# Performance work log

Measured on AMD Instinct MI355X. Metric: run time of the kernel, lower is better.

## Reference

```python
import jax, jax.numpy as jnp
import numpy as np

# Dims: B=4, C_in=256, H=W=64 -> L=4096, token_dim D=256, state_dim N=512, K=4
B_, C_IN, H_, W_ = 4, 256, 64, 64
D, N, K = 256, 512, 4


def setup_inputs() -> dict:
    key = jax.random.key(0)
    ks = jax.random.split(key, 16)
    g = lambda k, shape, sc=0.02: (jax.random.normal(k, shape, jnp.float32) * sc)
    return {
        'feat_map': jax.random.normal(ks[0], (B_, C_IN, H_, W_), jnp.float32),
        'hf_map':   jax.random.normal(ks[1], (B_, C_IN, H_, W_), jnp.float32),
        # 1x1 conv proj_f / proj_hf: weight (out=D, in=C_IN), bias (D,)
        'Wf':  g(ks[2], (D, C_IN)), 'bf':  jnp.zeros((D,), jnp.float32),
        'Whf': g(ks[3], (D, C_IN)), 'bhf': jnp.zeros((D,), jnp.float32),
        # alpha_head: Linear(D, D//2) -> GELU -> Linear(D//2, K)
        'Wa1': g(ks[4], (D // 2, D)), 'ba1': jnp.zeros((D // 2,), jnp.float32),
        'Wa2': g(ks[5], (K, D // 2)), 'ba2': jnp.zeros((K,), jnp.float32),
        # SelectiveSSM base tuples: diagonal decay logits A (K,N), input maps B (K,N,D), output maps C (K,D,N)
        'A_base': g(ks[6], (K, N), 1.0),
        'B_base': g(ks[7], (K, N, D), 0.02),
        'C_base': g(ks[8], (K, D, N), 0.02),
        # out_proj 1x1 conv: (C_IN, D)
        'Wout': g(ks[9], (C_IN, D)), 'bout': jnp.zeros((C_IN,), jnp.float32),
    }


def _stage(feat_map, hf_map, Wf, bf, Whf, bhf, Wa1, ba1, Wa2, ba2,
           A_base, B_base, C_base, Wout, bout):
    B, C, H, W = feat_map.shape
    L = H * W
    # 1x1 conv token projections -> (B, L, D)
    t_f = jnp.einsum('bchw,dc->bdhw', feat_map, Wf) + bf[None, :, None, None]
    t_hf = jnp.einsum('bchw,dc->bdhw', hf_map, Whf) + bhf[None, :, None, None]
    x = t_f.reshape(B, -1, L).transpose(0, 2, 1)        # (B, L, D)
    t_hf_seq = t_hf.reshape(B, -1, L).transpose(0, 2, 1)  # (B, L, D)
    # gating MLP -> per-token mixture weights over K base SSMs
    hmid = jax.nn.gelu(t_hf_seq @ Wa1.T + ba1, approximate=False)
    alpha = jax.nn.softmax(hmid @ Wa2.T + ba2, axis=-1)  # (B, L, K)
    # selective SSM: per-token mixed diagonal decay and input drive
    a = jax.nn.sigmoid(jnp.einsum('blk,kn->bln', alpha, A_base))   # (B, L, N)
    u = jnp.einsum('bld,blk,knd->bln', x, alpha, B_base)           # (B, L, N)

    def step(h, au):
        a_t, u_t = au                   # each (B, N)
        h = a_t * h + u_t
        return h, h

    h0 = jnp.zeros((B, a.shape[-1]), x.dtype)
    _, hs = jax.lax.scan(step, h0, (a.transpose(1, 0, 2), u.transpose(1, 0, 2)))
    h_seq = hs.transpose(1, 0, 2)                                   # (B, L, N)
    # mixed readout
    y = jnp.einsum('blk,bln,kdn->bld', alpha, h_seq, C_base)        # (B, L, D)
    y_map = y.transpose(0, 2, 1).reshape(B, -1, H, W)
    out = jnp.einsum('bdhw,cd->bchw', y_map, Wout) + bout[None, :, None, None]
    return out


def reference(feat_map, hf_map, Wf, bf, Whf, bhf, Wa1, ba1, Wa2, ba2,
              A_base, B_base, C_base, Wout, bout):
    return _stage(feat_map, hf_map, Wf, bf, Whf, bhf, Wa1, ba1, Wa2, ba2,
                  A_base, B_base, C_base, Wout, bout)
```

## Files before the change

kernel.cpp:

```cpp
#include <hip/hip_runtime.h>
#include <hip/hip_bf16.h>
#include <math.h>

#define B_  4
#define CIN 256
#define L_  4096
#define D_  256
#define N_  512
#define K_  4
#define DH  128
#define BL  (B_ * L_)

#define NCHUNK 128
#define CLEN   (L_ / NCHUNK)

typedef __attribute__((ext_vector_type(8))) short bfrag;
typedef __attribute__((ext_vector_type(4))) float f4;

__device__ __forceinline__ float bf2f(unsigned short u) {
  return __uint_as_float(((unsigned int)u) << 16);
}
__device__ __forceinline__ unsigned short f2bf(float f) {
  unsigned int u = __float_as_uint(f);
  return (unsigned short)((u + 0x7FFFu + ((u >> 16) & 1u)) >> 16);
}

__global__ void k_prep(const float* __restrict__ Wf, const float* __restrict__ Whf,
                       const float* __restrict__ Wa1, const float* __restrict__ Wout,
                       const float* __restrict__ Bb, const float* __restrict__ Cb,
                       const float* __restrict__ bfv, const float* __restrict__ bhfv,
                       unsigned short* __restrict__ Wfb ,
                       unsigned short* __restrict__ Wa1b,
                       unsigned short* __restrict__ Woutb,
                       unsigned short* __restrict__ Bb16,
                       unsigned short* __restrict__ Cb16,
                       float* __restrict__ biascat) {
  int i = blockIdx.x * 256 + threadIdx.x;
  if (i < 65536) { Wfb[i] = f2bf(Wf[i]); return; } i -= 65536;
  if (i < 65536) { Wfb[65536 + i] = f2bf(Whf[i]); return; } i -= 65536;
  if (i < 32768) { Wa1b[i] = f2bf(Wa1[i]); return; } i -= 32768;
  if (i < 65536) { Woutb[i] = f2bf(Wout[i]); return; } i -= 65536;
  if (i < 524288) {
    int d = i & 255, n = (i >> 8) & 511, k = i >> 17;
    Bb16[(((size_t)n << 2) | k) << 8 | d] = f2bf(Bb[i]);
    return;
  } i -= 524288;
  if (i < 524288) {
    int nn = i & 511, d = (i >> 9) & 255, k = i >> 17;
    Cb16[(((size_t)d << 2) | k) << 9 | nn] = f2bf(Cb[i]);
    return;
  } i -= 524288;
  if (i < 256) { biascat[i] = bfv[i]; return; } i -= 256;
  if (i < 256) { biascat[256 + i] = bhfv[i]; }
}

__global__ void k_transpose2(const float* __restrict__ feat, const float* __restrict__ hf,
                             unsigned short* __restrict__ featT ) {
  __shared__ float tile[32][33];
  const int z = blockIdx.z;
  const int b = z & 3, which = z >> 2;
  const float* in = which ? hf : feat;
  unsigned short* outT = featT + (size_t)which * BL * CIN;
  const int l0 = blockIdx.x * 32, c0 = blockIdx.y * 32;
  const int tx = threadIdx.x, ty = threadIdx.y;
  const float* p = in + ((size_t)b * CIN + c0 + ty) * L_ + l0 + tx;
#pragma unroll
  for (int i = 0; i < 32; i += 8) tile[ty + i][tx] = p[(size_t)i * L_];
  __syncthreads();
  unsigned short* q = outT + ((size_t)b * L_ + l0 + ty) * CIN + c0 + tx;
#pragma unroll
  for (int i = 0; i < 32; i += 8) q[(size_t)i * CIN] = f2bf(tile[tx][ty + i]);
}


__global__ void k_scanA(const unsigned short* __restrict__ u, const float* __restrict__ alpha,
                        const float* __restrict__ Abase,
                        float* __restrict__ P, float* __restrict__ Hend) {
  const int n = threadIdx.x;
  const int bc = blockIdx.x;
  const int b = bc >> 7, c = bc & 127;
  const float A0 = Abase[n], A1 = Abase[N_ + n], A2 = Abase[2 * N_ + n], A3 = Abase[3 * N_ + n];
  const size_t tok0 = (size_t)b * L_ + (size_t)c * CLEN;
  float p = 1.f, h = 0.f;
  for (int l = 0; l < CLEN; ++l) {
    const size_t t = tok0 + l;
    float4 al = *(const float4*)(alpha + t * 4);
    float s = al.x * A0 + al.y * A1 + al.z * A2 + al.w * A3;
    float av = 1.f / (1.f + expf(-s));
    float uv = bf2f(u[t * N_ + n]);
    h = av * h + uv;
    p *= av;
  }
  P[(size_t)bc * N_ + n] = p;
  Hend[(size_t)bc * N_ + n] = h;
}

__global__ void k_scanB(const float* __restrict__ P, const float* __restrict__ Hend,
                        float* __restrict__ Hstart) {
  const int n = threadIdx.x;
  const int b = blockIdx.x;
  float h = 0.f;
  for (int c = 0; c < NCHUNK; ++c) {
    size_t idx = ((size_t)b * NCHUNK + c) * N_ + n;
    Hstart[idx] = h;
    h = P[idx] * h + Hend[idx];
  }
}

__global__ void k_scanC(const unsigned short* __restrict__ u, const float* __restrict__ alpha,
                        const float* __restrict__ Abase, const float* __restrict__ Hstart,
                        unsigned short* __restrict__ hbf) {
  const int n = threadIdx.x;
  const int bc = blockIdx.x;
  const int b = bc >> 7, c = bc & 127;
  const float A0 = Abase[n], A1 = Abase[N_ + n], A2 = Abase[2 * N_ + n], A3 = Abase[3 * N_ + n];
  const size_t tok0 = (size_t)b * L_ + (size_t)c * CLEN;
  float h = Hstart[(size_t)bc * N_ + n];
  for (int l = 0; l < CLEN; ++l) {
    const size_t t = tok0 + l;
    float4 al = *(const float4*)(alpha + t * 4);
    float s = al.x * A0 + al.y * A1 + al.z * A2 + al.w * A3;
    float av = 1.f / (1.f + expf(-s));
    float uv = bf2f(u[t * N_ + n]);
    h = av * h + uv;
    hbf[t * N_ + n] = f2bf(h);
  }
}

#define BM 128
#define BN 128
#define BK 32

#define GLL(src, dst)                                                                      \
  __builtin_amdgcn_global_load_lds((const __attribute__((address_space(1))) void*)(src),   \
                                   (__attribute__((address_space(3))) void*)(dst), 16, 0, 0)

#define BM2 128
#define BN2 256

template <int BIAS, int EPI>
__global__ __launch_bounds__(512, 2) void gemm_bt2(
    const unsigned short* __restrict__ A, long sA,
    const unsigned short* __restrict__ Bm, long sB,
    const float* __restrict__ bias, long bS,
    const float* __restrict__ alphaP,
    void* __restrict__ Cv, long sC,
    int M, int N, int Kd, int lda, int ldb) {
  const int zb = blockIdx.z;
  A += (size_t)zb * sA;
  Bm += (size_t)zb * sB;
  if (BIAS) bias += (size_t)zb * bS;
  const int m0 = blockIdx.x * BM2;
  const int n0 = blockIdx.y * BN2;
  __shared__ __attribute__((aligned(16))) unsigned short As[2 * BM2 * BK];
  __shared__ __attribute__((aligned(16))) unsigned short Bs[2 * BN2 * BK];
  const int t = threadIdx.x;
  const int lane = t & 63;
  const int w = t >> 6;
  const int wm = (w >> 2) * 64;
  const int wn = (w & 3) * 64;

  f4 acc[4][4];
#pragma unroll
  for (int i = 0; i < 4; ++i)
#pragma unroll
    for (int j = 0; j < 4; ++j) acc[i][j] = (f4){0.f, 0.f, 0.f, 0.f};

  const int rS = t >> 2;
  const int cS = (((t & 3) ^ ((t >> 3) & 3))) * 8;
  const unsigned short* gA = A + (size_t)(m0 + rS) * lda + cS;
  const unsigned short* gB = Bm + (size_t)(n0 + rS) * ldb + cS;
  const long rowStepB = (long)128 * ldb;
  const int r16 = lane & 15;
  const int sx = (r16 >> 1) & 3;
  const int kg = (((lane >> 4) ^ sx)) * 8;

#define STAGE2(slot, kt)                                                \
  do {                                                                  \
    const unsigned short* sA_ = gA + (size_t)(kt) * BK;                 \
    const unsigned short* sB_ = gB + (size_t)(kt) * BK;                 \
    unsigned short* dA_ = As + (slot) * (BM2 * BK) + t * 8;             \
    unsigned short* dB_ = Bs + (slot) * (BN2 * BK) + t * 8;             \
    GLL(sA_, dA_);                                                      \
    GLL(sB_, dB_);                                                      \
    GLL(sB_ + rowStepB, dB_ + BM2 * BK);                                \
  } while (0)

  const int nIter = Kd / BK;
  STAGE2(0, 0);
  int cur = 0;
  for (int kt = 0; kt < nIter; ++kt) {
    asm volatile("s_waitcnt vmcnt(0)" ::: "memory");
    __builtin_amdgcn_s_barrier();
    asm volatile("" ::: "memory");
    if (kt + 1 < nIter) STAGE2(cur ^ 1, kt + 1);
    const unsigned short* Ab = As + cur * (BM2 * BK);
    const unsigned short* Bb2 = Bs + cur * (BN2 * BK);
    bfrag af[4], bfr[4];
#pragma unroll
    for (int i = 0; i < 4; ++i) {
      af[i]  = *(const bfrag*)(Ab + (wm + i * 16 + r16) * BK + kg);
      bfr[i] = *(const bfrag*)(Bb2 + (wn + i * 16 + r16) * BK + kg);
    }
    __builtin_amdgcn_s_setprio(1);
#pragma unroll
    for (int i = 0; i < 4; ++i)
#pragma unroll
      for (int j = 0; j < 4; ++j)
        acc[i][j] = __builtin_amdgcn_mfma_f32_16x16x32_bf16(af[i], bfr[j], acc[i][j], 0, 0, 0);
    __builtin_amdgcn_s_setprio(0);
    asm volatile("" ::: "memory");
    cur ^= 1;
  }
#undef STAGE2

  const int rowBase = m0 + wm + ((lane >> 4) << 2);
  const int colBase = n0 + wn + (lane & 15);

  if (EPI >= 2) {
    const int kq = lane & 3;
    const int NO = N >> 2;
    float av[4][4];
#pragma unroll
    for (int i = 0; i < 4; ++i)
#pragma unroll
      for (int r = 0; r < 4; ++r)
        av[i][r] = alphaP[(size_t)(rowBase + i * 16 + r) * 4 + kq];
    float* Cf = (float*)Cv + (size_t)zb * sC;
    unsigned short* Cb = (unsigned short*)Cv + (size_t)zb * sC;
#pragma unroll
    for (int i = 0; i < 4; ++i)
#pragma unroll
      for (int j = 0; j < 4; ++j) {
        const int col = colBase + j * 16;
#pragma unroll
        for (int r = 0; r < 4; ++r) {
          float p = av[i][r] * acc[i][j][r];
          p += __shfl_xor(p, 1);
          p += __shfl_xor(p, 2);
          if (kq == 0) {
            const int row = rowBase + i * 16 + r;
            if (EPI == 2) Cf[(size_t)row * NO + (col >> 2)] = p;
            else          Cb[(size_t)row * NO + (col >> 2)] = f2bf(p);
          }
        }
      }
    return;
  }

  float* Cf = (float*)Cv + (size_t)zb * sC;
  unsigned short* Cb = (unsigned short*)Cv + (size_t)zb * sC;
#pragma unroll
  for (int i = 0; i < 4; ++i) {
#pragma unroll
    for (int j = 0; j < 4; ++j) {
      const int col = colBase + j * 16;
#pragma unroll
      for (int r = 0; r < 4; ++r) {
        const int row = rowBase + i * 16 + r;
        float v = acc[i][j][r];
        if (BIAS == 1) v += bias[col];
        if (BIAS == 2) v += bias[row];
        if (EPI == 1) Cb[(size_t)row * N + col] = f2bf(v);
        else          Cf[(size_t)row * N + col] = v;
      }
    }
  }
}

template <int BIAS, int EPI >
__global__ __launch_bounds__(512, 2) void gemm_w8(
    const unsigned short* __restrict__ A, long sA,
    const unsigned short* __restrict__ Bm, long sB,
    const float* __restrict__ bias, long bS,
    void* __restrict__ Cv, long sC,
    int M, int N, int Kd, int lda, int ldb) {
  const int zb = blockIdx.z;
  A += (size_t)zb * sA;
  Bm += (size_t)zb * sB;
  if (BIAS) bias += (size_t)zb * bS;
  const int m0 = blockIdx.x * BM;
  const int n0 = blockIdx.y * BN;
  __shared__ __attribute__((aligned(16))) unsigned short As[3 * BM * BK];
  __shared__ __attribute__((aligned(16))) unsigned short Bs[3 * BN * BK];
  const int t = threadIdx.x;
  const int lane = t & 63;
  const int w = t >> 6;
  const int wm = (w >> 2) * 64;
  const int wn = (w & 3) * 32;

  f4 acc[4][2];
#pragma unroll
  for (int i = 0; i < 4; ++i)
#pragma unroll
    for (int j = 0; j < 2; ++j) acc[i][j] = (f4){0.f, 0.f, 0.f, 0.f};

  const int rS = t >> 2;
  const int cS = (((t & 3) ^ ((t >> 3) & 3))) * 8;
  const unsigned short* gA = A + (size_t)(m0 + rS) * lda + cS;
  const unsigned short* gB = Bm + (size_t)(n0 + rS) * ldb + cS;
  const int r16 = lane & 15;
  const int sx = (r16 >> 1) & 3;
  const int kg = (((lane >> 4) ^ sx)) * 8;

#define STAGEW(slot, kt)                                                \
  do {                                                                  \
    GLL(gA + (size_t)(kt) * BK, As + (slot) * (BM * BK) + t * 8);       \
    GLL(gB + (size_t)(kt) * BK, Bs + (slot) * (BN * BK) + t * 8);       \
  } while (0)

  const int nIter = Kd / BK;
  STAGEW(0, 0);
  STAGEW(1, 1);
  int slot = 0;
  for (int kt = 0; kt < nIter; ++kt) {
    if (kt + 1 < nIter) asm volatile("s_waitcnt vmcnt(2)" ::: "memory");
    else                asm volatile("s_waitcnt vmcnt(0)" ::: "memory");
    __builtin_amdgcn_s_barrier();
    asm volatile("" ::: "memory");
    if (kt + 2 < nIter) {
      int s2 = slot + 2; if (s2 >= 3) s2 -= 3;
      STAGEW(s2, kt + 2);
    }
    const unsigned short* Ab = As + slot * (BM * BK);
    const unsigned short* Bb2 = Bs + slot * (BN * BK);
    bfrag af[4], bfr[2];
#pragma unroll
    for (int i = 0; i < 4; ++i)
      af[i]  = *(const bfrag*)(Ab + (wm + i * 16 + r16) * BK + kg);
#pragma unroll
    for (int j = 0; j < 2; ++j)
      bfr[j] = *(const bfrag*)(Bb2 + (wn + j * 16 + r16) * BK + kg);
    __builtin_amdgcn_s_setprio(1);
#pragma unroll
    for (int i = 0; i < 4; ++i)
#pragma unroll
      for (int j = 0; j < 2; ++j)
        acc[i][j] = __builtin_amdgcn_mfma_f32_16x16x32_bf16(af[i], bfr[j], acc[i][j], 0, 0, 0);
    __builtin_amdgcn_s_setprio(0);
    asm volatile("" ::: "memory");
    slot = (slot == 2) ? 0 : slot + 1;
  }
#undef STAGEW

  const int rowBase = m0 + wm + ((lane >> 4) << 2);
  const int colBase = n0 + wn + (lane & 15);
  float* Cf = (float*)Cv + (size_t)zb * sC;
  unsigned short* Cb = (unsigned short*)Cv + (size_t)zb * sC;
#pragma unroll
  for (int i = 0; i < 4; ++i) {
#pragma unroll
    for (int j = 0; j < 2; ++j) {
      const int col = colBase + j * 16;
#pragma unroll
      for (int r = 0; r < 4; ++r) {
        const int row = rowBase + i * 16 + r;
        float v = acc[i][j][r];
        if (BIAS == 1) v += bias[col];
        if (BIAS == 2) v += bias[row];
        if (EPI == 1) Cb[(size_t)row * N + col] = f2bf(v);
        else          Cf[(size_t)row * N + col] = v;
      }
    }
  }
}

__global__ __launch_bounds__(512, 2) void gemm_alpha(
    const unsigned short* __restrict__ A,
    const unsigned short* __restrict__ Bm,
    const float* __restrict__ ba1, const float* __restrict__ Wa2,
    const float* __restrict__ ba2, float* __restrict__ alphaOut) {
  __shared__ __attribute__((aligned(16))) unsigned short smem[6 * BM * BK + 1344];
  unsigned short* As = smem;
  unsigned short* Bs = smem + 3 * BM * BK;
  unsigned short* tile = smem;
  float* w2s = (float*)(smem + 6 * BM * BK);
  float* b1s = w2s + 512;
  float* b2s = b1s + 128;
  const int t = threadIdx.x;
  const int lane = t & 63;
  const int w = t >> 6;
  const int wm = (w >> 2) * 64;
  const int wn = (w & 3) * 32;
  const int m0 = blockIdx.x * BM;

  f4 acc[4][2];
#pragma unroll
  for (int i = 0; i < 4; ++i)
#pragma unroll
    for (int j = 0; j < 2; ++j) acc[i][j] = (f4){0.f, 0.f, 0.f, 0.f};

  const int rS = t >> 2;
  const int cS = (((t & 3) ^ ((t >> 3) & 3))) * 8;
  const unsigned short* gA = A + (size_t)(m0 + rS) * D_ + cS;
  const unsigned short* gB = Bm + (size_t)rS * D_ + cS;
  const int r16 = lane & 15;
  const int sx = (r16 >> 1) & 3;
  const int kg = (((lane >> 4) ^ sx)) * 8;

#define STAGEA(slot, kt)                                                \
  do {                                                                  \
    GLL(gA + (size_t)(kt) * BK, As + (slot) * (BM * BK) + t * 8);       \
    GLL(gB + (size_t)(kt) * BK, Bs + (slot) * (BM * BK) + t * 8);       \
  } while (0)

  const int nIter = D_ / BK;
  STAGEA(0, 0);
  STAGEA(1, 1);
  int slot = 0;
  for (int kt = 0; kt < nIter; ++kt) {
    if (kt + 1 < nIter) asm volatile("s_waitcnt vmcnt(2)" ::: "memory");
    else                asm volatile("s_waitcnt vmcnt(0)" ::: "memory");
    __builtin_amdgcn_s_barrier();
    asm volatile("" ::: "memory");
    if (kt + 2 < nIter) {
      int s2 = slot + 2; if (s2 >= 3) s2 -= 3;
      STAGEA(s2, kt + 2);
    }
    const unsigned short* Ab = As + slot * (BM * BK);
    const unsigned short* Bb2 = Bs + slot * (BM * BK);
    bfrag af[4], bfr[2];
#pragma unroll
    for (int i = 0; i < 4; ++i)
      af[i]  = *(const bfrag*)(Ab + (wm + i * 16 + r16) * BK + kg);
#pragma unroll
    for (int j = 0; j < 2; ++j)
      bfr[j] = *(const bfrag*)(Bb2 + (wn + j * 16 + r16) * BK + kg);
    __builtin_amdgcn_s_setprio(1);
#pragma unroll
    for (int i = 0; i < 4; ++i)
#pragma unroll
      for (int j = 0; j < 2; ++j)
        acc[i][j] = __builtin_amdgcn_mfma_f32_16x16x32_bf16(af[i], bfr[j], acc[i][j], 0, 0, 0);
    __builtin_amdgcn_s_setprio(0);
    asm volatile("" ::: "memory");
    slot = (slot == 2) ? 0 : slot + 1;
  }
#undef STAGEA

  __syncthreads();
  w2s[t & 511] = Wa2[t & 511];
  if (t < DH) b1s[t] = ba1[t];
  if (t < K_) b2s[t] = ba2[t];
  const int lrowBase = wm + ((lane >> 4) << 2);
  const int lcolBase = wn + r16;
#pragma unroll
  for (int i = 0; i < 4; ++i)
#pragma unroll
    for (int j = 0; j < 2; ++j) {
      const int col = lcolBase + j * 16;
#pragma unroll
      for (int r = 0; r < 4; ++r)
        tile[(lrowBase + i * 16 + r) * DH + col] = f2bf(acc[i][j][r]);
    }
  __syncthreads();

  const int tok = t >> 2;
  const int q = t & 3;
  float a0 = 0.f, a1 = 0.f, a2 = 0.f, a3 = 0.f;
#pragma unroll 8
  for (int e = 0; e < 32; ++e) {
    const int d = q * 32 + e;
    float g = bf2f(tile[tok * DH + d]) + b1s[d];
    g = 0.5f * g * (1.0f + erff(g * 0.70710678118654752f));
    a0 += g * w2s[0 * DH + d];
    a1 += g * w2s[1 * DH + d];
    a2 += g * w2s[2 * DH + d];
    a3 += g * w2s[3 * DH + d];
  }
  a0 += __shfl_xor(a0, 1); a1 += __shfl_xor(a1, 1); a2 += __shfl_xor(a2, 1); a3 += __shfl_xor(a3, 1);
  a0 += __shfl_xor(a0, 2); a1 += __shfl_xor(a1, 2); a2 += __shfl_xor(a2, 2); a3 += __shfl_xor(a3, 2);
  a0 += b2s[0]; a1 += b2s[1]; a2 += b2s[2]; a3 += b2s[3];
  float m = fmaxf(fmaxf(a0, a1), fmaxf(a2, a3));
  float e0 = expf(a0 - m), e1 = expf(a1 - m), e2 = expf(a2 - m), e3 = expf(a3 - m);
  float inv = 1.f / (e0 + e1 + e2 + e3);
  float my = (q == 0) ? e0 : (q == 1) ? e1 : (q == 2) ? e2 : e3;
  alphaOut[(size_t)(m0 + tok) * 4 + q] = my * inv;
}


extern "C" void kernel_launch(void* const* d_in, const int* in_sizes, int n_in,
                              void* d_out, int out_size, void* d_ws, size_t ws_size,
                              hipStream_t stream) {
  const float* feat  = (const float*)d_in[0];
  const float* hf    = (const float*)d_in[1];
  const float* Wf    = (const float*)d_in[2];
  const float* bfv   = (const float*)d_in[3];
  const float* Whf   = (const float*)d_in[4];
  const float* bhfv  = (const float*)d_in[5];
  const float* Wa1   = (const float*)d_in[6];
  const float* ba1   = (const float*)d_in[7];
  const float* Wa2   = (const float*)d_in[8];
  const float* ba2   = (const float*)d_in[9];
  const float* Abase = (const float*)d_in[10];
  const float* Bbase = (const float*)d_in[11];
  const float* Cbase = (const float*)d_in[12];
  const float* Wout  = (const float*)d_in[13];
  const float* bout  = (const float*)d_in[14];
  float* out = (float*)d_out;

  char* ws = (char*)d_ws;
  size_t off = 0;
  auto alloc = [&](size_t bytes) { void* p = ws + off; off += bytes; return p; };

  unsigned short* Wfb    = (unsigned short*)alloc((size_t)2 * D_ * CIN * 2);
  unsigned short* Wa1b   = (unsigned short*)alloc((size_t)DH * D_ * 2);
  unsigned short* Woutb  = (unsigned short*)alloc((size_t)CIN * D_ * 2);
  unsigned short* Bb16   = (unsigned short*)alloc((size_t)K_ * N_ * D_ * 2);
  unsigned short* Cb16   = (unsigned short*)alloc((size_t)K_ * D_ * N_ * 2);
  float*          biascat= (float*)alloc((size_t)2 * D_ * 4);
  float*          alpha  = (float*)alloc((size_t)BL * K_ * 4);
  float*          Pc     = (float*)alloc((size_t)B_ * NCHUNK * N_ * 4);
  float*          He     = (float*)alloc((size_t)B_ * NCHUNK * N_ * 4);
  float*          Hs     = (float*)alloc((size_t)B_ * NCHUNK * N_ * 4);
  unsigned short* hbf    = (unsigned short*)alloc((size_t)BL * N_ * 2);
  unsigned short* x      = (unsigned short*)alloc((size_t)BL * D_ * 2);
  unsigned short* thf    = (unsigned short*)alloc((size_t)BL * D_ * 2);
  unsigned short* featT  = (unsigned short*)alloc((size_t)BL * CIN * 2);
  unsigned short* hfT    = (unsigned short*)alloc((size_t)BL * CIN * 2);
  unsigned short* u16    = (unsigned short*)alloc((size_t)BL * N_ * 2);

  unsigned short* y   = thf;

  if (ws_size < off) return;

  k_prep<<<dim3((3 * 65536 + 32768 + 2 * 524288 + 512 + 255) / 256), 256, 0, stream>>>(
      Wf, Whf, Wa1, Wout, Bbase, Cbase, bfv, bhfv, Wfb, Wa1b, Woutb, Bb16, Cb16, biascat);

  k_transpose2<<<dim3(L_ / 32, CIN / 32, 2 * B_), dim3(32, 8), 0, stream>>>(feat, hf, featT);

  gemm_w8<1, 1><<<dim3(BL / BM, D_ / BN, 2), 512, 0, stream>>>(
      featT, (long)BL * CIN, Wfb, (long)D_ * CIN, biascat, D_,
      x, (long)BL * D_, BL, D_, CIN, CIN, CIN);

  gemm_alpha<<<dim3(BL / BM), 512, 0, stream>>>(thf, Wa1b, ba1, Wa2, ba2, alpha);

  gemm_bt2<0, 3><<<dim3(BL / BM2, (K_ * N_) / BN2, 1), 512, 0, stream>>>(
      x, 0, Bb16, 0, nullptr, 0, alpha, u16, 0, BL, K_ * N_, D_, D_, D_);

  k_scanA<<<dim3(B_ * NCHUNK), N_, 0, stream>>>(u16, alpha, Abase, Pc, He);
  k_scanB<<<dim3(B_), N_, 0, stream>>>(Pc, He, Hs);
  k_scanC<<<dim3(B_ * NCHUNK), N_, 0, stream>>>(u16, alpha, Abase, Hs, hbf);

  gemm_bt2<0, 3><<<dim3(BL / BM2, (K_ * D_) / BN2, 1), 512, 0, stream>>>(
      hbf, 0, Cb16, 0, nullptr, 0, alpha, y, 0, BL, K_ * D_, N_, N_, N_);

  gemm_w8<2, 0><<<dim3(CIN / BM, L_ / BN, B_), 512, 0, stream>>>(
      Woutb, 0, y, (long)L_ * D_, bout, 0, out, (long)CIN * L_, CIN, L_, D_, D_, D_);
}
```

Measured before the change: 139.9 us.

## Fold output projection into C readout weights and fuse transposed NCHW epilogue

Precomputes the combined weights Wout·C_k for each of the K bases (a small weight-only GEMM), so the readout GEMM directly produces output channels instead of the intermediate y. That removes the separate out_proj GEMM and the y round-trip. The new EPI==4 epilogue reduces over K with alpha, stages the tile in shared memory, transposes it to NCHW layout, and adds the bias with vectorized stores. This adds a per-call weight transpose and GEMM, and the folded weights get an extra bf16 rounding.

```diff
diff --git a/kernel.cpp b/kernel.cpp
--- a/kernel.cpp
+++ b/kernel.cpp
@@ -27,13 +27,12 @@
 
 __global__ void k_prep(const float* __restrict__ Wf, const float* __restrict__ Whf,
                        const float* __restrict__ Wa1, const float* __restrict__ Wout,
-                       const float* __restrict__ Bb, const float* __restrict__ Cb,
+                       const float* __restrict__ Bb,
                        const float* __restrict__ bfv, const float* __restrict__ bhfv,
                        unsigned short* __restrict__ Wfb ,
                        unsigned short* __restrict__ Wa1b,
                        unsigned short* __restrict__ Woutb,
                        unsigned short* __restrict__ Bb16,
-                       unsigned short* __restrict__ Cb16,
                        float* __restrict__ biascat) {
   int i = blockIdx.x * 256 + threadIdx.x;
   if (i < 65536) { Wfb[i] = f2bf(Wf[i]); return; } i -= 65536;
@@ -45,13 +44,22 @@
     Bb16[(((size_t)n << 2) | k) << 8 | d] = f2bf(Bb[i]);
     return;
   } i -= 524288;
-  if (i < 524288) {
-    int nn = i & 511, d = (i >> 9) & 255, k = i >> 17;
-    Cb16[(((size_t)d << 2) | k) << 9 | nn] = f2bf(Cb[i]);
-    return;
-  } i -= 524288;
   if (i < 256) { biascat[i] = bfv[i]; return; } i -= 256;
   if (i < 256) { biascat[256 + i] = bhfv[i]; }
+}
+
+__global__ void k_transC(const float* __restrict__ Cb, unsigned short* __restrict__ Ct16) {
+  __shared__ float tile[32][33];
+  const int k = blockIdx.z;
+  const int d0 = blockIdx.x * 32, n0 = blockIdx.y * 32;
+  const int tx = threadIdx.x, ty = threadIdx.y;
+  const float* p = Cb + ((size_t)k * D_ + d0 + ty) * N_ + n0 + tx;
+#pragma unroll
+  for (int i = 0; i < 32; i += 8) tile[ty + i][tx] = p[(size_t)i * N_];
+  __syncthreads();
+  unsigned short* q = Ct16 + ((size_t)k * N_ + n0 + ty) * D_ + d0 + tx;
+#pragma unroll
+  for (int i = 0; i < 32; i += 8) q[(size_t)i * D_] = f2bf(tile[tx][ty + i]);
 }
 
 __global__ void k_transpose2(const float* __restrict__ feat, const float* __restrict__ hf,
@@ -216,9 +224,48 @@
 
   const int rowBase = m0 + wm + ((lane >> 4) << 2);
   const int colBase = n0 + wn + (lane & 15);
-
-  if (EPI >= 2) {
-    const int kq = lane & 3;
+  const int kq = lane & 3;
+
+  if (EPI == 4) {
+    float av[4][4];
+#pragma unroll
+    for (int i = 0; i < 4; ++i)
+#pragma unroll
+      for (int r = 0; r < 4; ++r)
+        av[i][r] = alphaP[(size_t)(rowBase + i * 16 + r) * 4 + kq];
+    __syncthreads();
+    float* T = (float*)Bs;
+#pragma unroll
+    for (int i = 0; i < 4; ++i)
+#pragma unroll
+      for (int j = 0; j < 4; ++j) {
+        const int col = colBase + j * 16;
+#pragma unroll
+        for (int r = 0; r < 4; ++r) {
+          float p = av[i][r] * acc[i][j][r];
+          p += __shfl_xor(p, 1);
+          p += __shfl_xor(p, 2);
+          if (kq == 0) T[((col - n0) >> 2) * 128 + (rowBase + i * 16 + r - m0)] = p;
+        }
+      }
+    __syncthreads();
+    const int b = m0 >> 12;
+    const int l0 = m0 & (L_ - 1);
+    const int cb2 = n0 >> 2;
+    const int cl = t >> 3;
+    const int lo = (t & 7) * 16;
+    float* op = (float*)Cv + (size_t)b * CIN * L_ + (size_t)(cb2 + cl) * L_ + l0 + lo;
+    const float bo = bias[cb2 + cl];
+#pragma unroll
+    for (int v4 = 0; v4 < 4; ++v4) {
+      float4 q = *(const float4*)(T + cl * 128 + lo + v4 * 4);
+      q.x += bo; q.y += bo; q.z += bo; q.w += bo;
+      *(float4*)(op + v4 * 4) = q;
+    }
+    return;
+  }
+
+  if (EPI == 3) {
     const int NO = N >> 2;
     float av[4][4];
 #pragma unroll
@@ -226,7 +273,6 @@
 #pragma unroll
       for (int r = 0; r < 4; ++r)
         av[i][r] = alphaP[(size_t)(rowBase + i * 16 + r) * 4 + kq];
-    float* Cf = (float*)Cv + (size_t)zb * sC;
     unsigned short* Cb = (unsigned short*)Cv + (size_t)zb * sC;
 #pragma unroll
     for (int i = 0; i < 4; ++i)
@@ -240,31 +286,11 @@
           p += __shfl_xor(p, 2);
           if (kq == 0) {
             const int row = rowBase + i * 16 + r;
-            if (EPI == 2) Cf[(size_t)row * NO + (col >> 2)] = p;
-            else          Cb[(size_t)row * NO + (col >> 2)] = f2bf(p);
+            Cb[(size_t)row * NO + (col >> 2)] = f2bf(p);
           }
         }
       }
     return;
-  }
-
-  float* Cf = (float*)Cv + (size_t)zb * sC;
-  unsigned short* Cb = (unsigned short*)Cv + (size_t)zb * sC;
-#pragma unroll
-  for (int i = 0; i < 4; ++i) {
-#pragma unroll
-    for (int j = 0; j < 4; ++j) {
-      const int col = colBase + j * 16;
-#pragma unroll
-      for (int r = 0; r < 4; ++r) {
-        const int row = rowBase + i * 16 + r;
-        float v = acc[i][j][r];
-        if (BIAS == 1) v += bias[col];
-        if (BIAS == 2) v += bias[row];
-        if (EPI == 1) Cb[(size_t)row * N + col] = f2bf(v);
-        else          Cf[(size_t)row * N + col] = v;
-      }
-    }
   }
 }
 
@@ -274,7 +300,7 @@
     const unsigned short* __restrict__ Bm, long sB,
     const float* __restrict__ bias, long bS,
     void* __restrict__ Cv, long sC,
-    int M, int N, int Kd, int lda, int ldb) {
+    int M, int N, int Kd, int lda, int ldb, int ldc) {
   const int zb = blockIdx.z;
   A += (size_t)zb * sA;
   Bm += (size_t)zb * sB;
@@ -358,8 +384,8 @@
         float v = acc[i][j][r];
         if (BIAS == 1) v += bias[col];
         if (BIAS == 2) v += bias[row];
-        if (EPI == 1) Cb[(size_t)row * N + col] = f2bf(v);
-        else          Cf[(size_t)row * N + col] = v;
+        if (EPI == 1) Cb[(size_t)row * ldc + col] = f2bf(v);
+        else          Cf[(size_t)row * ldc + col] = v;
       }
     }
   }
@@ -507,7 +533,8 @@
   unsigned short* Wa1b   = (unsigned short*)alloc((size_t)DH * D_ * 2);
   unsigned short* Woutb  = (unsigned short*)alloc((size_t)CIN * D_ * 2);
   unsigned short* Bb16   = (unsigned short*)alloc((size_t)K_ * N_ * D_ * 2);
-  unsigned short* Cb16   = (unsigned short*)alloc((size_t)K_ * D_ * N_ * 2);
+  unsigned short* Ct16   = (unsigned short*)alloc((size_t)K_ * N_ * D_ * 2);
+  unsigned short* CWcat  = (unsigned short*)alloc((size_t)K_ * CIN * N_ * 2);
   float*          biascat= (float*)alloc((size_t)2 * D_ * 4);
   float*          alpha  = (float*)alloc((size_t)BL * K_ * 4);
   float*          Pc     = (float*)alloc((size_t)B_ * NCHUNK * N_ * 4);
@@ -520,18 +547,19 @@
   unsigned short* hfT    = (unsigned short*)alloc((size_t)BL * CIN * 2);
   unsigned short* u16    = (unsigned short*)alloc((size_t)BL * N_ * 2);
 
-  unsigned short* y   = thf;
-
   if (ws_size < off) return;
 
-  k_prep<<<dim3((3 * 65536 + 32768 + 2 * 524288 + 512 + 255) / 256), 256, 0, stream>>>(
-      Wf, Whf, Wa1, Wout, Bbase, Cbase, bfv, bhfv, Wfb, Wa1b, Woutb, Bb16, Cb16, biascat);
+  k_prep<<<dim3((3 * 65536 + 32768 + 524288 + 512 + 255) / 256), 256, 0, stream>>>(
+      Wf, Whf, Wa1, Wout, Bbase, bfv, bhfv, Wfb, Wa1b, Woutb, Bb16, biascat);
+  k_transC<<<dim3(D_ / 32, N_ / 32, K_), dim3(32, 8), 0, stream>>>(Cbase, Ct16);
+  gemm_w8<0, 1><<<dim3(CIN / BM, N_ / BN, K_), 512, 0, stream>>>(
+      Woutb, 0, Ct16, (long)N_ * D_, nullptr, 0, CWcat, N_, CIN, N_, D_, D_, D_, K_ * N_);
 
   k_transpose2<<<dim3(L_ / 32, CIN / 32, 2 * B_), dim3(32, 8), 0, stream>>>(feat, hf, featT);
 
   gemm_w8<1, 1><<<dim3(BL / BM, D_ / BN, 2), 512, 0, stream>>>(
       featT, (long)BL * CIN, Wfb, (long)D_ * CIN, biascat, D_,
-      x, (long)BL * D_, BL, D_, CIN, CIN, CIN);
+      x, (long)BL * D_, BL, D_, CIN, CIN, CIN, D_);
 
   gemm_alpha<<<dim3(BL / BM), 512, 0, stream>>>(thf, Wa1b, ba1, Wa2, ba2, alpha);
 
@@ -542,9 +570,6 @@
   k_scanB<<<dim3(B_), N_, 0, stream>>>(Pc, He, Hs);
   k_scanC<<<dim3(B_ * NCHUNK), N_, 0, stream>>>(u16, alpha, Abase, Hs, hbf);
 
-  gemm_bt2<0, 3><<<dim3(BL / BM2, (K_ * D_) / BN2, 1), 512, 0, stream>>>(
-      hbf, 0, Cb16, 0, nullptr, 0, alpha, y, 0, BL, K_ * D_, N_, N_, N_);
-
-  gemm_w8<2, 0><<<dim3(CIN / BM, L_ / BN, B_), 512, 0, stream>>>(
-      Woutb, 0, y, (long)L_ * D_, bout, 0, out, (long)CIN * L_, CIN, L_, D_, D_, D_);
-}
+  gemm_bt2<0, 4><<<dim3(BL / BM2, (K_ * CIN) / BN2, 1), 512, 0, stream>>>(
+      hbf, 0, CWcat, 0, bout, 0, alpha, out, 0, BL, K_ * CIN, N_, N_, N_);
+}
```

New measurement: 147.0 us. +5.1%, slower.
